# Optimization experiments

Measured on AMD Instinct MI355X. Metric: run time of the kernel, lower is better.

Reference implementation:

```python
import jax, jax.numpy as jnp
import numpy as np

N, F = 4096, 256
EPS = 1e-12

def _prep_P(P):
    # replicate __init__ preprocessing: symmetrize, normalize, *4, clamp, /4
    P = P + P.T
    P = P / np.sum(P)
    P = P * 4
    P = np.maximum(P, 1e-12)
    P = P / 4
    return P


def setup_inputs() -> dict:
    key = jax.random.key(0)
    k1, k2, k3, k4, k5 = jax.random.split(key, 5)
    rng = np.random.default_rng(0)
    P1 = jnp.asarray(_prep_P(rng.uniform(size=(N, N)).astype(np.float32)))
    P2 = jnp.asarray(_prep_P(rng.uniform(size=(N, N)).astype(np.float32)))
    X1 = jax.random.normal(k1, (N, F), dtype=jnp.float32)
    X2 = jax.random.normal(k2, (N, F), dtype=jnp.float32)
    W = jax.random.uniform(k3, (1, F), dtype=jnp.float32)
    return {"P1": P1, "P2": P2, "X1": X1, "X2": X2, "W": W}


def _batch_loss(P, X, W):
    Y = X * W                                  # [N, F]
    sq = jnp.sum(Y * Y, axis=1)                # [N]
    # squared euclidean distance via mm (matches cdist use_mm_for_euclid_dist, then squared)
    d2 = jnp.maximum(sq[:, None] + sq[None, :] - 2.0 * (Y @ Y.T), 0.0)  # [N, N]
    temp = 1.0 / (1.0 + d2)                    # t-distribution kernel
    n = temp.shape[0]
    diag = jnp.eye(n, dtype=bool)
    temp = jnp.where(diag, 0.0, temp)
    Q = jnp.maximum(temp / jnp.sum(temp), EPS)
    kl = jnp.where(diag, 0.0, P * jnp.log(P / Q))
    return jnp.sum(kl)


def reference(P1, P2, X1, X2, W):
    loss = _batch_loss(P1, X1, W) + _batch_loss(P2, X2, W)
    return loss / 2.0
```

## Files before the change

kernel.cpp:

```cpp
#include <hip/hip_runtime.h>
#include <math.h>

#define N 4096
#define F 256
#define NT 32
#define BM 128
#define BK 32

typedef short short8 __attribute__((ext_vector_type(8)));
typedef float f32x4  __attribute__((ext_vector_type(4)));

typedef const __attribute__((address_space(1))) unsigned int guint_t;
typedef __attribute__((address_space(3))) unsigned int luint_t;

__device__ __forceinline__ void gload_lds16(const void* g, void* l) {
    __builtin_amdgcn_global_load_lds((guint_t*)g, (luint_t*)l, 16, 0, 0);
}

__device__ __forceinline__ unsigned short f2bf(float x) {
    unsigned u = __float_as_uint(x);
    unsigned r = (u + 0x7fff + ((u >> 16) & 1)) >> 16;
    return (unsigned short)r;
}
__device__ __forceinline__ float bf2f(unsigned short x) {
    return __uint_as_float(((unsigned)x) << 16);
}

__global__ __launch_bounds__(256)
void prep_kernel(const float* __restrict__ X1, const float* __restrict__ X2,
                 const float* __restrict__ W,
                 unsigned short* __restrict__ Yhi, unsigned short* __restrict__ Ylo,
                 float* __restrict__ sqg)
{
    const int t = threadIdx.x;
    const int rid0 = blockIdx.x * 8;
    const float w = W[t];
    __shared__ float red[8][4];
    const int lane = t & 63, wv = t >> 6;
    #pragma unroll
    for (int r = 0; r < 8; ++r) {
        int rid = rid0 + r;
        int b = rid >> 12, row = rid & (N - 1);
        const float* X = b ? X2 : X1;
        float y = X[(size_t)row * F + t] * w;
        unsigned short h = f2bf(y);
        float lf = y - bf2f(h);
        size_t off = (size_t)rid * F + t;
        Yhi[off] = h;
        Ylo[off] = f2bf(lf);
        float s = y * y;
        #pragma unroll
        for (int o = 32; o > 0; o >>= 1) s += __shfl_down(s, o);
        if (lane == 0) red[r][wv] = s;
    }
    __syncthreads();
    if (t < 8) {
        sqg[rid0 + t] = red[t][0] + red[t][1] + red[t][2] + red[t][3];
    }
}

__global__ __launch_bounds__(256)
void tsne_tile_kernel(const unsigned short* __restrict__ Yhi,
                      const unsigned short* __restrict__ Ylo,
                      const float* __restrict__ sqg,
                      const float* __restrict__ P1, const float* __restrict__ P2,
                      double* __restrict__ pS, double* __restrict__ pA,
                      double* __restrict__ pB)
{
    int bx = blockIdx.x, by = blockIdx.y, bz = blockIdx.z;
    int pidx = bz * (NT * NT) + by * NT + bx;
    if (bx < by) {
        if (threadIdx.x == 0) { pS[pidx] = 0.0; pA[pidx] = 0.0; pB[pidx] = 0.0; }
        return;
    }
    const float* P  = bz ? P2 : P1;
    const unsigned short* Ah = Yhi + (size_t)bz * N * F;
    const unsigned short* Al = Ylo + (size_t)bz * N * F;
    const float* sq = sqg + bz * N;
    const float wgt = (bx == by) ? 1.0f : 2.0f;

    __shared__ unsigned short sbuf[2][4][BM * BK];

    const int t = threadIdx.x;
    const int lane = t & 63, w = t >> 6;
    const int wx = w & 1, wy = w >> 1;

    f32x4 acc[4][4];
    #pragma unroll
    for (int fm = 0; fm < 4; ++fm)
        #pragma unroll
        for (int fn = 0; fn < 4; ++fn) acc[fm][fn] = (f32x4){0.f, 0.f, 0.f, 0.f};

    const int arow = by * BM, brow = bx * BM;
    const int c = lane >> 4, mr = lane & 15;

#define STAGE(db, k0)                                                      \
    {                                                                      \
        _Pragma("unroll")                                                  \
        for (int it = 0; it < 2; ++it) {                                   \
            int cid = it * 256 + w * 64 + lane;                            \
            int row = cid >> 2;                                            \
            int kl  = cid & 3;                                             \
            int kg  = kl ^ ((row >> 1) & 3);                               \
            int ldsoff = (it * 256 + w * 64) * 8;                          \
            size_t ga = (size_t)(arow + row) * F + (k0) + kg * 8;          \
            size_t gb = (size_t)(brow + row) * F + (k0) + kg * 8;          \
            gload_lds16(Ah + ga, &sbuf[db][0][ldsoff]);                    \
            gload_lds16(Al + ga, &sbuf[db][1][ldsoff]);                    \
            gload_lds16(Ah + gb, &sbuf[db][2][ldsoff]);                    \
            gload_lds16(Al + gb, &sbuf[db][3][ldsoff]);                    \
        }                                                                  \
    }

    STAGE(0, 0);
    __syncthreads();

    for (int ks = 0; ks < F / BK; ++ks) {
        const int db = ks & 1;
        if (ks < F / BK - 1) STAGE(db ^ 1, (ks + 1) * BK);

        short8 ah[4], al[4], bh[4], bl[4];
        #pragma unroll
        for (int fm = 0; fm < 4; ++fm) {
            int row = wy * 64 + fm * 16 + mr;
            int ad = row * BK + ((c ^ ((row >> 1) & 3)) * 8);
            ah[fm] = *(const short8*)&sbuf[db][0][ad];
            al[fm] = *(const short8*)&sbuf[db][1][ad];
        }
        #pragma unroll
        for (int fn = 0; fn < 4; ++fn) {
            int row = wx * 64 + fn * 16 + mr;
            int ad = row * BK + ((c ^ ((row >> 1) & 3)) * 8);
            bh[fn] = *(const short8*)&sbuf[db][2][ad];
            bl[fn] = *(const short8*)&sbuf[db][3][ad];
        }
        #pragma unroll
        for (int fm = 0; fm < 4; ++fm)
            #pragma unroll
            for (int fn = 0; fn < 4; ++fn) {
                acc[fm][fn] = __builtin_amdgcn_mfma_f32_16x16x32_bf16(ah[fm], bh[fn], acc[fm][fn], 0, 0, 0);
                acc[fm][fn] = __builtin_amdgcn_mfma_f32_16x16x32_bf16(ah[fm], bl[fn], acc[fm][fn], 0, 0, 0);
                acc[fm][fn] = __builtin_amdgcn_mfma_f32_16x16x32_bf16(al[fm], bh[fn], acc[fm][fn], 0, 0, 0);
            }
        __syncthreads();
    }
#undef STAGE

    const int q = lane >> 4, nn = lane & 15;
    const int gi0 = arow + wy * 64, gj0 = brow + wx * 64;
    float sp = 0.f, ap = 0.f, bp = 0.f;
    #pragma unroll
    for (int fm = 0; fm < 4; ++fm) {
        float sqi[4];
        #pragma unroll
        for (int r = 0; r < 4; ++r) sqi[r] = sq[gi0 + fm * 16 + q * 4 + r];
        #pragma unroll
        for (int fn = 0; fn < 4; ++fn) {
            int j = gj0 + fn * 16 + nn;
            float sqj = sq[j];
            #pragma unroll
            for (int r = 0; r < 4; ++r) {
                int i = gi0 + fm * 16 + q * 4 + r;
                float one_d2 = 1.0f + fmaxf(sqi[r] + sqj - 2.0f * acc[fm][fn][r], 0.0f);
                if (i != j) {
                    float p = P[(size_t)i * N + j];
                    sp += __builtin_amdgcn_rcpf(one_d2);
                    ap += p * __logf(p * one_d2);
                    bp += p;
                }
            }
        }
    }
    sp *= wgt; ap *= wgt; bp *= wgt;

    #pragma unroll
    for (int o = 32; o > 0; o >>= 1) {
        sp += __shfl_down(sp, o);
        ap += __shfl_down(ap, o);
        bp += __shfl_down(bp, o);
    }
    float* red = (float*)&sbuf[0][0][0];
    if (lane == 0) { red[w] = sp; red[4 + w] = ap; red[8 + w] = bp; }
    __syncthreads();
    if (t == 0) {
        pS[pidx] = (double)(red[0] + red[1] + red[2] + red[3]);
        pA[pidx] = (double)(red[4] + red[5] + red[6] + red[7]);
        pB[pidx] = (double)(red[8] + red[9] + red[10] + red[11]);
    }
}

__global__ __launch_bounds__(256)
void finish_kernel(const double* __restrict__ pS, const double* __restrict__ pA,
                   const double* __restrict__ pB, float* __restrict__ out)
{
    int t = threadIdx.x;
    double s0 = 0, a0 = 0, b0 = 0, s1 = 0, a1 = 0, b1 = 0;
    for (int i = t; i < NT * NT; i += 256) {
        s0 += pS[i];           a0 += pA[i];           b0 += pB[i];
        s1 += pS[i + NT * NT]; a1 += pA[i + NT * NT]; b1 += pB[i + NT * NT];
    }
    __shared__ double red[6][256];
    red[0][t] = s0; red[1][t] = a0; red[2][t] = b0;
    red[3][t] = s1; red[4][t] = a1; red[5][t] = b1;
    __syncthreads();
    for (int o = 128; o > 0; o >>= 1) {
        if (t < o) {
            #pragma unroll
            for (int qd = 0; qd < 6; ++qd) red[qd][t] += red[qd][t + o];
        }
        __syncthreads();
    }
    if (t == 0) {
        double kl1 = red[1][0] + red[2][0] * log(red[0][0]);
        double kl2 = red[4][0] + red[5][0] * log(red[3][0]);
        out[0] = (float)((kl1 + kl2) * 0.5);
    }
}

extern "C" void kernel_launch(void* const* d_in, const int* in_sizes, int n_in,
                              void* d_out, int out_size, void* d_ws, size_t ws_size,
                              hipStream_t stream)
{
    const float* P1 = (const float*)d_in[0];
    const float* P2 = (const float*)d_in[1];
    const float* X1 = (const float*)d_in[2];
    const float* X2 = (const float*)d_in[3];
    const float* W  = (const float*)d_in[4];
    float* out = (float*)d_out;

    unsigned short* Yhi = (unsigned short*)d_ws;
    unsigned short* Ylo = Yhi + (size_t)2 * N * F;
    float* sq = (float*)(Ylo + (size_t)2 * N * F);
    double* pS = (double*)(sq + 2 * N);
    double* pA = pS + 2 * NT * NT;
    double* pB = pA + 2 * NT * NT;

    prep_kernel<<<(2 * N) / 8, 256, 0, stream>>>(X1, X2, W, Yhi, Ylo, sq);
    tsne_tile_kernel<<<dim3(NT, NT, 2), 256, 0, stream>>>(Yhi, Ylo, sq,
                                                          P1, P2, pS, pA, pB);
    finish_kernel<<<1, 256, 0, stream>>>(pS, pA, pB, out);
}
```

Baseline: 221.9 us.

## Launch only upper-triangle tiles, single-buffer LDS, raise occupancy with XCD-aware mapping

Replaces the 32x32x2 grid, whose lower-triangle blocks exited early, with a compact 1D grid of 1056 workgroups covering only upper-triangle tiles. Block ids are remapped so consecutive blocks spread round-robin across the 8 XCDs. LDS drops from double to single buffering and launch bounds request 5 waves per SIMD, trading global-to-LDS prefetch overlap for higher occupancy. A serial loop recovers the tile coordinates, and the finish kernel now reduces over the 528 triangle tiles.

```diff
diff --git a/kernel.cpp b/kernel.cpp
--- a/kernel.cpp
+++ b/kernel.cpp
@@ -6,6 +6,8 @@
 #define NT 32
 #define BM 128
 #define BK 32
+#define NTRI 528
+#define NWG  1056
 
 typedef short short8 __attribute__((ext_vector_type(8)));
 typedef float f32x4  __attribute__((ext_vector_type(4)));
@@ -59,7 +61,7 @@
     }
 }
 
-__global__ __launch_bounds__(256)
+__global__ __launch_bounds__(256, 5)
 void tsne_tile_kernel(const unsigned short* __restrict__ Yhi,
                       const unsigned short* __restrict__ Ylo,
                       const float* __restrict__ sqg,
@@ -67,19 +69,20 @@
                       double* __restrict__ pS, double* __restrict__ pA,
                       double* __restrict__ pB)
 {
-    int bx = blockIdx.x, by = blockIdx.y, bz = blockIdx.z;
-    int pidx = bz * (NT * NT) + by * NT + bx;
-    if (bx < by) {
-        if (threadIdx.x == 0) { pS[pidx] = 0.0; pA[pidx] = 0.0; pB[pidx] = 0.0; }
-        return;
-    }
+    const int wg  = (blockIdx.x & 7) * 132 + (blockIdx.x >> 3);
+    const int bz  = wg >= NTRI;
+    int r = wg - bz * NTRI;
+    int by = 0;
+    while (r >= NT - by) { r -= NT - by; ++by; }
+    const int bx = by + r;
+
     const float* P  = bz ? P2 : P1;
     const unsigned short* Ah = Yhi + (size_t)bz * N * F;
     const unsigned short* Al = Ylo + (size_t)bz * N * F;
     const float* sq = sqg + bz * N;
     const float wgt = (bx == by) ? 1.0f : 2.0f;
 
-    __shared__ unsigned short sbuf[2][4][BM * BK];
+    __shared__ unsigned short sbuf[4][BM * BK];
 
     const int t = threadIdx.x;
     const int lane = t & 63, w = t >> 6;
@@ -94,45 +97,38 @@
     const int arow = by * BM, brow = bx * BM;
     const int c = lane >> 4, mr = lane & 15;
 
-#define STAGE(db, k0)                                                      \
-    {                                                                      \
-        _Pragma("unroll")                                                  \
-        for (int it = 0; it < 2; ++it) {                                   \
-            int cid = it * 256 + w * 64 + lane;                            \
-            int row = cid >> 2;                                            \
-            int kl  = cid & 3;                                             \
-            int kg  = kl ^ ((row >> 1) & 3);                               \
-            int ldsoff = (it * 256 + w * 64) * 8;                          \
-            size_t ga = (size_t)(arow + row) * F + (k0) + kg * 8;          \
-            size_t gb = (size_t)(brow + row) * F + (k0) + kg * 8;          \
-            gload_lds16(Ah + ga, &sbuf[db][0][ldsoff]);                    \
-            gload_lds16(Al + ga, &sbuf[db][1][ldsoff]);                    \
-            gload_lds16(Ah + gb, &sbuf[db][2][ldsoff]);                    \
-            gload_lds16(Al + gb, &sbuf[db][3][ldsoff]);                    \
-        }                                                                  \
-    }
-
-    STAGE(0, 0);
-    __syncthreads();
-
     for (int ks = 0; ks < F / BK; ++ks) {
-        const int db = ks & 1;
-        if (ks < F / BK - 1) STAGE(db ^ 1, (ks + 1) * BK);
+        const int k0 = ks * BK;
+        #pragma unroll
+        for (int it = 0; it < 2; ++it) {
+            int cid = it * 256 + w * 64 + lane;
+            int row = cid >> 2;
+            int kl  = cid & 3;
+            int kg  = kl ^ ((row >> 1) & 3);
+            int ldsoff = (it * 256 + w * 64) * 8;
+            size_t ga = (size_t)(arow + row) * F + k0 + kg * 8;
+            size_t gb = (size_t)(brow + row) * F + k0 + kg * 8;
+            gload_lds16(Ah + ga, &sbuf[0][ldsoff]);
+            gload_lds16(Al + ga, &sbuf[1][ldsoff]);
+            gload_lds16(Ah + gb, &sbuf[2][ldsoff]);
+            gload_lds16(Al + gb, &sbuf[3][ldsoff]);
+        }
+        __syncthreads();
 
         short8 ah[4], al[4], bh[4], bl[4];
         #pragma unroll
         for (int fm = 0; fm < 4; ++fm) {
             int row = wy * 64 + fm * 16 + mr;
             int ad = row * BK + ((c ^ ((row >> 1) & 3)) * 8);
-            ah[fm] = *(const short8*)&sbuf[db][0][ad];
-            al[fm] = *(const short8*)&sbuf[db][1][ad];
+            ah[fm] = *(const short8*)&sbuf[0][ad];
+            al[fm] = *(const short8*)&sbuf[1][ad];
         }
         #pragma unroll
         for (int fn = 0; fn < 4; ++fn) {
             int row = wx * 64 + fn * 16 + mr;
             int ad = row * BK + ((c ^ ((row >> 1) & 3)) * 8);
-            bh[fn] = *(const short8*)&sbuf[db][2][ad];
-            bl[fn] = *(const short8*)&sbuf[db][3][ad];
+            bh[fn] = *(const short8*)&sbuf[2][ad];
+            bl[fn] = *(const short8*)&sbuf[3][ad];
         }
         #pragma unroll
         for (int fm = 0; fm < 4; ++fm)
@@ -144,7 +140,6 @@
             }
         __syncthreads();
     }
-#undef STAGE
 
     const int q = lane >> 4, nn = lane & 15;
     const int gi0 = arow + wy * 64, gj0 = brow + wx * 64;
@@ -153,15 +148,15 @@
     for (int fm = 0; fm < 4; ++fm) {
         float sqi[4];
         #pragma unroll
-        for (int r = 0; r < 4; ++r) sqi[r] = sq[gi0 + fm * 16 + q * 4 + r];
+        for (int rr = 0; rr < 4; ++rr) sqi[rr] = sq[gi0 + fm * 16 + q * 4 + rr];
         #pragma unroll
         for (int fn = 0; fn < 4; ++fn) {
             int j = gj0 + fn * 16 + nn;
             float sqj = sq[j];
             #pragma unroll
-            for (int r = 0; r < 4; ++r) {
-                int i = gi0 + fm * 16 + q * 4 + r;
-                float one_d2 = 1.0f + fmaxf(sqi[r] + sqj - 2.0f * acc[fm][fn][r], 0.0f);
+            for (int rr = 0; rr < 4; ++rr) {
+                int i = gi0 + fm * 16 + q * 4 + rr;
+                float one_d2 = 1.0f + fmaxf(sqi[rr] + sqj - 2.0f * acc[fm][fn][rr], 0.0f);
                 if (i != j) {
                     float p = P[(size_t)i * N + j];
                     sp += __builtin_amdgcn_rcpf(one_d2);
@@ -179,13 +174,13 @@
         ap += __shfl_down(ap, o);
         bp += __shfl_down(bp, o);
     }
-    float* red = (float*)&sbuf[0][0][0];
+    float* red = (float*)&sbuf[0][0];
     if (lane == 0) { red[w] = sp; red[4 + w] = ap; red[8 + w] = bp; }
     __syncthreads();
     if (t == 0) {
-        pS[pidx] = (double)(red[0] + red[1] + red[2] + red[3]);
-        pA[pidx] = (double)(red[4] + red[5] + red[6] + red[7]);
-        pB[pidx] = (double)(red[8] + red[9] + red[10] + red[11]);
+        pS[wg] = (double)(red[0] + red[1] + red[2] + red[3]);
+        pA[wg] = (double)(red[4] + red[5] + red[6] + red[7]);
+        pB[wg] = (double)(red[8] + red[9] + red[10] + red[11]);
     }
 }
 
@@ -195,9 +190,9 @@
 {
     int t = threadIdx.x;
     double s0 = 0, a0 = 0, b0 = 0, s1 = 0, a1 = 0, b1 = 0;
-    for (int i = t; i < NT * NT; i += 256) {
-        s0 += pS[i];           a0 += pA[i];           b0 += pB[i];
-        s1 += pS[i + NT * NT]; a1 += pA[i + NT * NT]; b1 += pB[i + NT * NT];
+    for (int i = t; i < NTRI; i += 256) {
+        s0 += pS[i];        a0 += pA[i];        b0 += pB[i];
+        s1 += pS[i + NTRI]; a1 += pA[i + NTRI]; b1 += pB[i + NTRI];
     }
     __shared__ double red[6][256];
     red[0][t] = s0; red[1][t] = a0; red[2][t] = b0;
@@ -232,11 +227,10 @@
     unsigned short* Ylo = Yhi + (size_t)2 * N * F;
     float* sq = (float*)(Ylo + (size_t)2 * N * F);
     double* pS = (double*)(sq + 2 * N);
-    double* pA = pS + 2 * NT * NT;
-    double* pB = pA + 2 * NT * NT;
+    double* pA = pS + NWG;
+    double* pB = pA + NWG;
 
     prep_kernel<<<(2 * N) / 8, 256, 0, stream>>>(X1, X2, W, Yhi, Ylo, sq);
-    tsne_tile_kernel<<<dim3(NT, NT, 2), 256, 0, stream>>>(Yhi, Ylo, sq,
-                                                          P1, P2, pS, pA, pB);
+    tsne_tile_kernel<<<NWG, 256, 0, stream>>>(Yhi, Ylo, sq, P1, P2, pS, pA, pB);
     finish_kernel<<<1, 256, 0, stream>>>(pS, pA, pB, out);
 }
```

New measurement: 277.5 us. +25.1%, slower.
